# Performance work log

Measured on AMD Instinct MI355X. Metric: run time of the kernel, lower is better.

## Reference

```python
import jax, jax.numpy as jnp
import numpy as np
from jax import lax

EPS = 1e-5

def _conv(x, w, pad):
    return lax.conv_general_dilated(x, w, (1, 1), [(pad, pad), (pad, pad)],
                                    dimension_numbers=('NCHW', 'OIHW', 'NCHW'))

def _bn(x, g, b, m, v):
    inv = g * jax.lax.rsqrt(v + EPS)
    return x * inv[None, :, None, None] + (b - m * inv)[None, :, None, None]

def _deform(x, ow, ob):
    # ConvOffset2d: 3x3 conv predicts 2*C per-channel (dy,dx) offsets, then
    # bilinear resample each channel at (grid + offset), clipped to the image.
    B, C, H, W = x.shape
    off = _conv(x, ow, 1) + ob[None, :, None, None]          # [B,2C,H,W]
    off = off.reshape(B, C, 2, H, W)
    yy = jnp.arange(H, dtype=x.dtype)[:, None]
    xx = jnp.arange(W, dtype=x.dtype)[None, :]
    py = jnp.clip(yy + off[:, :, 0], 0.0, H - 1)             # [B,C,H,W]
    px = jnp.clip(xx + off[:, :, 1], 0.0, W - 1)
    y0 = jnp.floor(py).astype(jnp.int32)
    x0 = jnp.floor(px).astype(jnp.int32)
    y1 = jnp.minimum(y0 + 1, H - 1)
    x1 = jnp.minimum(x0 + 1, W - 1)
    wy = py - y0.astype(x.dtype)
    wx = px - x0.astype(x.dtype)
    flat = x.reshape(B, C, H * W)
    def g(yi, xi):
        idx = (yi * W + xi).reshape(B, C, H * W)
        return jnp.take_along_axis(flat, idx, axis=2).reshape(B, C, H, W)
    v00, v01, v10, v11 = g(y0, x0), g(y0, x1), g(y1, x0), g(y1, x1)
    return (v00 * (1 - wy) * (1 - wx) + v01 * (1 - wy) * wx +
            v10 * wy * (1 - wx) + v11 * wy * wx)

def setup_inputs() -> dict:
    key = jax.random.key(0)
    ks = jax.random.split(key, 32)
    B, Cin, Cmid, H, W = 4, 1024, 256, 64, 64
    d = {}
    d['x'] = jax.random.normal(ks[0], (B, Cin, H, W), jnp.float32)
    # offset-predicting convs (3x3, C -> 2C), small init so offsets ~O(1)
    d['ow1'] = jax.random.normal(ks[1], (2 * Cin, Cin, 3, 3), jnp.float32) * 0.01
    d['ob1'] = jnp.zeros((2 * Cin,), jnp.float32)
    d['ow2'] = jax.random.normal(ks[2], (2 * Cmid, Cmid, 3, 3), jnp.float32) * 0.01
    d['ob2'] = jnp.zeros((2 * Cmid,), jnp.float32)
    d['ow3'] = jax.random.normal(ks[3], (2 * Cmid, Cmid, 3, 3), jnp.float32) * 0.01
    d['ob3'] = jnp.zeros((2 * Cmid,), jnp.float32)
    # bottleneck convs (no bias, as in ResNet)
    d['w1'] = jax.random.normal(ks[4], (Cmid, Cin, 1, 1), jnp.float32) * (1.0 / np.sqrt(Cin))
    d['w2'] = jax.random.normal(ks[5], (Cmid, Cmid, 3, 3), jnp.float32) * (1.0 / np.sqrt(9 * Cmid))
    d['w3'] = jax.random.normal(ks[6], (Cin, Cmid, 1, 1), jnp.float32) * (1.0 / np.sqrt(Cmid))
    # batchnorm (inference) params
    for i, c in zip((1, 2, 3), (Cmid, Cmid, Cin)):
        d[f'g{i}'] = jnp.ones((c,), jnp.float32)
        d[f'b{i}'] = jnp.zeros((c,), jnp.float32)
        d[f'm{i}'] = jax.random.normal(ks[10 + i], (c,), jnp.float32) * 0.1
        d[f'v{i}'] = jnp.ones((c,), jnp.float32) + jax.random.uniform(ks[20 + i], (c,), jnp.float32) * 0.1
    return d

def reference(x, ow1, ob1, w1, g1, b1, m1, v1,
              ow2, ob2, w2, g2, b2, m2, v2,
              ow3, ob3, w3, g3, b3, m3, v3):
    h = _deform(x, ow1, ob1)
    h = _bn(_conv(h, w1, 0), g1, b1, m1, v1)
    h = _deform(h, ow2, ob2)
    h = _bn(_conv(h, w2, 1), g2, b2, m2, v2)
    h = _deform(h, ow3, ob3)
    h = _bn(_conv(h, w3, 0), g3, b3, m3, v3)
    return jax.nn.relu(h)
```

## Files before the change

### kernel.cpp

```cpp
#include <hip/hip_runtime.h>


typedef unsigned short u16;
typedef __bf16 bf16x8 __attribute__((ext_vector_type(8)));
typedef float f32x4 __attribute__((ext_vector_type(4)));
typedef _Float16 f16;

__device__ __forceinline__ u16 f2bf(float f) {
  unsigned u = __float_as_uint(f);
  u += 0x7fffu + ((u >> 16) & 1u);
  return (u16)(u >> 16);
}
__device__ __forceinline__ float bf2f(u16 h) { return __uint_as_float((unsigned)h << 16); }
__device__ __forceinline__ u16 f2h(float f) { f16 h = (f16)f; return __builtin_bit_cast(u16, h); }
__device__ __forceinline__ float h2f(u16 u) { return (float)__builtin_bit_cast(f16, u); }

__device__ __forceinline__ void gload16(const u16* g, u16* l) {
  __builtin_amdgcn_global_load_lds((__attribute__((address_space(1))) unsigned int*)g,
                                   (__attribute__((address_space(3))) unsigned int*)l,
                                   16, 0, 0);
}

#define VM8() asm volatile("s_waitcnt vmcnt(8)" ::: "memory")
#define VM6() asm volatile("s_waitcnt vmcnt(6)" ::: "memory")
#define VM0() asm volatile("s_waitcnt vmcnt(0)" ::: "memory")
#define BAR()                                   \
  do {                                          \
    asm volatile("" ::: "memory");              \
    __builtin_amdgcn_s_barrier();               \
    asm volatile("" ::: "memory");              \
  } while (0)
#define LGK0()                                          \
  do {                                                  \
    asm volatile("s_waitcnt lgkmcnt(0)" ::: "memory");  \
    __builtin_amdgcn_sched_barrier(0);                  \
  } while (0)
#define SB0() __builtin_amdgcn_sched_barrier(0)

__global__ __launch_bounds__(256) void zero_k(uint4* __restrict__ p, unsigned n) {
  unsigned i = blockIdx.x * 256u + threadIdx.x;
  const unsigned st = gridDim.x * 256u;
  uint4 z; z.x = 0u; z.y = 0u; z.z = 0u; z.w = 0u;
  for (; i < n; i += st) p[i] = z;
}

template <int SPLIT>
__global__ __launch_bounds__(256) void pack_w(const float* __restrict__ w,
                                              u16* __restrict__ hi, u16* __restrict__ lo,
                                              int M, int C, int T) {
  const int AK = C * T;
  const int id = blockIdx.x * 256 + threadIdx.x;
  if (id >= M * AK) return;
  const int j = id & 7;
  const int slot = (id >> 3) & 511;
  const int rest = id >> 12;
  const int steps = AK >> 5;
  const int step = rest % steps;
  const int mt = rest / steps;
  const int kg = slot >> 7, m = slot & 127;
  const int k = step * 32 + kg * 8 + j;
  const int tap = k / C;
  const int c = k - tap * C;
  const int mg = mt * 128 + m;
  const float v = w[((size_t)mg * C + c) * T + tap];
  const u16 h = f2bf(v);
  hi[id] = h;
  if (SPLIT) lo[id] = f2bf(v - bf2f(h));
}

template <int CC, int T>
__global__ __launch_bounds__(256) void pack8_w(const float* __restrict__ w,
                                               u16* __restrict__ dst, int M) {
  constexpr int KT2 = 2 * (T * CC / 64);
  const int id = blockIdx.x * 256 + threadIdx.x;
  if (id >= M * CC * T) return;
  const int j = id & 7;
  const int d = (id >> 3) & 1023;
  const int rest = id >> 13;
  const int H = rest % KT2;
  const int mt = rest / KT2;
  const int row = d >> 2, kq = d & 3;
  const int k = H * 32 + ((kq ^ ((row >> 1) & 3)) * 8) + j;
  const int tap = k / CC, c = k - tap * CC;
  const int oc = mt * 256 + row;
  dst[id] = f2bf(w[((size_t)oc * CC + c) * T + tap]);
}

__global__ __launch_bounds__(256) void prep_x(const float* __restrict__ x,
                                              u16* __restrict__ xp) {
  __shared__ float t[64][65];
  const int c0 = blockIdx.x * 64;
  const int y = blockIdx.y;
  const int b = blockIdx.z;
  const int tid = threadIdx.x;
#pragma unroll
  for (int i = 0; i < 16; ++i) {
    const int idx = i * 256 + tid;
    const int ci = idx >> 6, xi = idx & 63;
    t[ci][xi] = x[(((size_t)b * 1024 + c0 + ci) * 64 + y) * 64 + xi];
  }
  __syncthreads();
#pragma unroll
  for (int i = 0; i < 16; ++i) {
    const int idx = i * 256 + tid;
    const int xi = idx >> 6, ci = idx & 63;
    xp[((size_t)((b * 66 + y + 1) * 66 + (xi + 1))) * 1024 + c0 + ci] = f2bf(t[ci][xi]);
  }
}

template <int C, int PADDST>
__global__ __launch_bounds__(256) void deform_k(const u16* __restrict__ src,
                                                const u16* __restrict__ off,
                                                u16* __restrict__ dst) {
  const int id = blockIdx.x * 256 + threadIdx.x;
  const int c = id & (C - 1);
  const int pix = id / C;
  const int b = pix >> 12;
  const int y = (pix >> 6) & 63;
  const int x = pix & 63;
  const unsigned ov = *(const unsigned*)(off + (size_t)pix * (2 * C) + 2 * c);
  const float py = fminf(fmaxf((float)y + h2f((u16)(ov & 0xffffu)), 0.f), 63.f);
  const float px = fminf(fmaxf((float)x + h2f((u16)(ov >> 16)), 0.f), 63.f);
  const int y0i = (int)py, x0i = (int)px;
  const int y1i = min(y0i + 1, 63), x1i = min(x0i + 1, 63);
  const float wy = py - (float)y0i, wx = px - (float)x0i;
  const int bb66 = b * 66;
  auto at = [&](int yi, int xi) -> size_t {
    return ((size_t)((bb66 + yi + 1) * 66 + (xi + 1))) * C + c;
  };
  const float v00 = bf2f(src[at(y0i, x0i)]);
  const float v01 = bf2f(src[at(y0i, x1i)]);
  const float v10 = bf2f(src[at(y1i, x0i)]);
  const float v11 = bf2f(src[at(y1i, x1i)]);
  const float val = v00 * (1.f - wy) * (1.f - wx) + v01 * (1.f - wy) * wx +
                    v10 * wy * (1.f - wx) + v11 * wy * wx;
  const size_t d = PADDST ? at(y, x) : (size_t)id;
  dst[d] = f2bf(val);
}

template <int TAPS, int CC, int NMT>
__global__ __launch_bounds__(512, 2) void gemm8_conv(
    const u16* __restrict__ Apack, const u16* __restrict__ Bsrc,
    const float* __restrict__ bias, u16* __restrict__ out, int M) {
  constexpr int KT = TAPS * CC / 64;
  constexpr int KT2 = 2 * KT;
  __shared__ u16 lds[65536];
  const int tid = threadIdx.x;
  const int w = tid >> 6, lane = tid & 63;
  const int wm = w >> 2, wn = w & 3;
  const int kg = lane >> 4, lm = lane & 15;
  const int g = blockIdx.x;
  const int local = g >> 3;
  const int mt = local % NMT;
  const int nt = (g & 7) * 8 + local / NMT;
  const int b_img = nt >> 4;
  const int y0 = (nt & 15) * 4;

  int laneA[2], laneB[2];
  unsigned ldsoff[2];
#pragma unroll
  for (int it = 0; it < 2; ++it) {
    const int d = it * 512 + tid;
    laneA[it] = d * 8;
    const int pl = d >> 2, kq = d & 3;
    const int r = pl >> 6, xc = pl & 63;
    laneB[it] = (r * 66 + xc) * CC + (kq ^ ((pl >> 1) & 3)) * 8;
    ldsoff[it] = (unsigned)(it * 512 + (tid & ~63)) * 8u;
  }
  const u16* Abase = Apack + (size_t)mt * KT2 * 8192;
  const u16* Bbase = Bsrc + (size_t)(b_img * 66 + y0) * 66 * CC;

  f32x4 acc[8][4];
  const f32x4 fz = {0.f, 0.f, 0.f, 0.f};
#pragma unroll
  for (int i = 0; i < 8; ++i)
#pragma unroll
    for (int j = 0; j < 4; ++j) acc[i][j] = fz;

  auto rbase = [&](int b, int op, int kh) -> unsigned {
    return (unsigned)(((b * 2 + op) * 2 + kh) * 8192);
  };
  auto stageA = [&](int H) {
    if (H >= KT2) return;
    const u16* p = Abase + (size_t)H * 8192;
    const unsigned db = rbase((H >> 1) & 1, 0, H & 1);
    gload16(p + laneA[0], (u16*)&lds[db + ldsoff[0]]);
    gload16(p + laneA[1], (u16*)&lds[db + ldsoff[1]]);
  };
  auto stageB = [&](int H) {
    if (H >= KT2) return;
    const int kglob = H * 32;
    const int tap = (TAPS == 1) ? 0 : (kglob / CC);
    const int cbase = kglob - tap * CC;
    const int ky = (TAPS == 9) ? tap / 3 : 0, kx = (TAPS == 9) ? tap % 3 : 0;
    const u16* p = Bbase + (ky * 66 + kx) * CC + cbase;
    const unsigned db = rbase((H >> 1) & 1, 1, H & 1);
    gload16(p + laneB[0], (u16*)&lds[db + ldsoff[0]]);
    gload16(p + laneB[1], (u16*)&lds[db + ldsoff[1]]);
  };

  bf16x8 afE[4], afO[4], bfA[4], bfB[4];
  auto rdA = [&](bf16x8* dst, int buf, int kh, int MG) {
    const unsigned regA = rbase(buf, 0, kh);
#pragma unroll
    for (int f = 0; f < 4; ++f) {
      const int row = wm * 128 + (MG * 4 + f) * 16 + lm;
      dst[f] = *(const bf16x8*)&lds[regA + row * 32 + (kg ^ ((row >> 1) & 3)) * 8];
    }
  };
  auto rdB = [&](bf16x8* dst, int buf, int kh) {
    const unsigned regB = rbase(buf, 1, kh);
#pragma unroll
    for (int f = 0; f < 4; ++f) {
      const int pc = wn * 64 + f * 16 + lm;
      dst[f] = *(const bf16x8*)&lds[regB + pc * 32 + (kg ^ ((pc >> 1) & 3)) * 8];
    }
  };

#define MFMA16(MG_, AF_, BF_)                                                        \
  do {                                                                               \
    __builtin_amdgcn_s_setprio(1);                                                   \
    _Pragma("unroll") for (int f = 0; f < 4; ++f)                                    \
        _Pragma("unroll") for (int nf = 0; nf < 4; ++nf)                             \
            acc[MG_ * 4 + f][nf] = __builtin_amdgcn_mfma_f32_16x16x32_bf16(          \
                AF_[f], BF_[nf], acc[MG_ * 4 + f][nf], 0, 0, 0);                     \
    __builtin_amdgcn_s_setprio(0);                                                   \
  } while (0)

  stageA(0); stageB(0);
  stageA(1); stageB(1);
  stageA(2); stageB(2);
  VM8();
  BAR();
  rdA(afE, 0, 0, 0);
  rdB(bfA, 0, 0);

  for (int t = 0; t < KT; ++t) {
    const int bi = t & 1;
    LGK0();
    rdA(afO, bi, 0, 1);
    stageA(2 * t + 3);
    SB0();
    MFMA16(0, afE, bfA);
    if (t >= KT - 2) VM0(); else VM6();
    BAR();
    LGK0();
    rdA(afE, bi, 1, 0);
    rdB(bfB, bi, 1);
    stageB(2 * t + 3);
    SB0();
    MFMA16(1, afO, bfA);
    BAR();
    LGK0();
    rdA(afO, bi, 1, 1);
    stageA(2 * t + 4);
    SB0();
    MFMA16(0, afE, bfB);
    if (t < KT - 2) VM6();
    BAR();
    LGK0();
    if (t + 1 < KT) {
      rdA(afE, bi ^ 1, 0, 0);
      rdB(bfA, bi ^ 1, 0);
    }
    stageB(2 * t + 4);
    SB0();
    MFMA16(1, afO, bfB);
    BAR();
  }
#undef MFMA16

  const int ocb = mt * 256 + wm * 128 + kg * 4;
#pragma unroll
  for (int mf = 0; mf < 8; ++mf) {
    const int oc0 = ocb + mf * 16;
    const f32x4 bv = *(const f32x4*)&bias[oc0];
#pragma unroll
    for (int nf = 0; nf < 4; ++nf) {
      const int pix = nt * 256 + wn * 64 + nf * 16 + lm;
      f32x4 r = acc[mf][nf] + bv;
      uint2 hv;
      hv.x = (unsigned)f2h(r[0]) | ((unsigned)f2h(r[1]) << 16);
      hv.y = (unsigned)f2h(r[2]) | ((unsigned)f2h(r[3]) << 16);
      *(uint2*)(out + (size_t)pix * M + oc0) = hv;
    }
  }
}

template <int TAPS, int PAD, int EPI, int CC, int WSPLIT>
__global__ __launch_bounds__(256, 2) void gemm_conv(
    const u16* __restrict__ Aph, const u16* __restrict__ Apl,
    const u16* __restrict__ Bh,
    const float* __restrict__ p0, const float* __restrict__ p1,
    const float* __restrict__ p2, const float* __restrict__ p3,
    float* __restrict__ outF, u16* __restrict__ o16a, int M) {
  constexpr int NB = 2 + WSPLIT;
  __shared__ u16 lds[NB * 4096];
  constexpr int steps = TAPS * (CC / 32);
  const int tid = threadIdx.x;
  const int w = tid >> 6, lane = tid & 63;
  const int wm = (w >> 1) * 64, wn = (w & 1) * 64;
  const int kg = lane >> 4, lm = lane & 15;
  const int wg = blockIdx.x;
  const int chunk = (int)(gridDim.x >> 3);
  const int g = (wg & 7) * chunk + (wg >> 3);
  const int mt = g >> 7, nt = g & 127;
  const int b_img = nt >> 5;
  const int y0 = (nt & 31) * 2;

  f32x4 acc[4][4];
  const f32x4 fz = {0.f, 0.f, 0.f, 0.f};
#pragma unroll
  for (int i = 0; i < 4; ++i)
#pragma unroll
    for (int j = 0; j < 4; ++j) acc[i][j] = fz;

  const u16* Abase_h = Aph + (size_t)mt * steps * 4096;
  const u16* Abase_l = WSPLIT ? (Apl + (size_t)mt * steps * 4096) : nullptr;

  for (int step = 0; step < steps; ++step) {
    const int tap = (TAPS == 1) ? 0 : (step / (CC / 32));
    const int c0 = (step - tap * (CC / 32)) * 32;
    const int ky = (TAPS == 9) ? (tap / 3) : 0;
    const int kx = (TAPS == 9) ? (tap % 3) : 0;

#pragma unroll
    for (int it = 0; it < 2; ++it) {
      const int slot = w * 128 + it * 64 + lane;
      const unsigned ldso = (unsigned)(w * 128 + it * 64) * 8u;
      const size_t ga = (size_t)step * 4096 + (size_t)slot * 8;
      gload16(Abase_h + ga, &lds[0 * 4096 + ldso]);
      if (WSPLIT) gload16(Abase_l + ga, &lds[1 * 4096 + ldso]);
      const int n = slot >> 2, kq = slot & 3;
      const int kga = kq ^ ((n >> 1) & 3);
      size_t gb;
      if (PAD) {
        const int r = n >> 6, xc = n & 63;
        gb = ((size_t)((b_img * 66 + (y0 + r + ky)) * 66 + (xc + kx))) * CC +
             (size_t)(c0 + kga * 8);
      } else {
        gb = (size_t)(nt * 128 + n) * CC + (size_t)(c0 + kga * 8);
      }
      gload16(Bh + gb, &lds[(NB - 1) * 4096 + ldso]);
    }
    __syncthreads();

    bf16x8 ah[4], al[4], bh[4];
#pragma unroll
    for (int f = 0; f < 4; ++f) {
      const unsigned ao = (unsigned)(kg * 128 + wm + f * 16 + lm) * 8u;
      ah[f] = *(const bf16x8*)&lds[0 * 4096 + ao];
      if (WSPLIT) al[f] = *(const bf16x8*)&lds[1 * 4096 + ao];
      const int n = wn + f * 16 + lm;
      const unsigned bo = (unsigned)(n * 4 + (kg ^ ((n >> 1) & 3))) * 8u;
      bh[f] = *(const bf16x8*)&lds[(NB - 1) * 4096 + bo];
    }
#pragma unroll
    for (int i = 0; i < 4; ++i)
#pragma unroll
      for (int j = 0; j < 4; ++j) {
        acc[i][j] = __builtin_amdgcn_mfma_f32_16x16x32_bf16(ah[i], bh[j], acc[i][j], 0, 0, 0);
        if (WSPLIT)
          acc[i][j] = __builtin_amdgcn_mfma_f32_16x16x32_bf16(al[i], bh[j], acc[i][j], 0, 0, 0);
      }
    __syncthreads();
  }

  const int ocb = mt * 128 + wm + kg * 4;
#pragma unroll
  for (int fi = 0; fi < 4; ++fi) {
    const int oc0 = ocb + fi * 16;
    f32x4 scl, sft;
    if (EPI == 0) {
#pragma unroll
      for (int j = 0; j < 4; ++j) { scl[j] = 1.f; sft[j] = p0[oc0 + j]; }
    } else {
#pragma unroll
      for (int j = 0; j < 4; ++j) {
        const float inv = p0[oc0 + j] / sqrtf(p3[oc0 + j] + 1e-5f);
        scl[j] = inv;
        sft[j] = p1[oc0 + j] - p2[oc0 + j] * inv;
      }
    }
#pragma unroll
    for (int fj = 0; fj < 4; ++fj) {
      const int pix = nt * 128 + wn + fj * 16 + lm;
      f32x4 r = acc[fi][fj] * scl + sft;
      if (EPI == 0) {
        uint2 hv;
        hv.x = (unsigned)f2h(r[0]) | ((unsigned)f2h(r[1]) << 16);
        hv.y = (unsigned)f2h(r[2]) | ((unsigned)f2h(r[3]) << 16);
        *(uint2*)(o16a + (size_t)pix * M + oc0) = hv;
      } else if (EPI == 1) {
        const int bb = pix >> 12, yy = (pix >> 6) & 63, xx = pix & 63;
        const size_t pp = ((size_t)((bb * 66 + yy + 1) * 66 + (xx + 1))) * M + oc0;
        uint2 hv;
        hv.x = (unsigned)f2bf(r[0]) | ((unsigned)f2bf(r[1]) << 16);
        hv.y = (unsigned)f2bf(r[2]) | ((unsigned)f2bf(r[3]) << 16);
        *(uint2*)(o16a + pp) = hv;
      } else {
        const int bb = pix >> 12, pin = pix & 4095;
#pragma unroll
        for (int j = 0; j < 4; ++j)
          outF[((size_t)(bb * M + oc0 + j)) * 4096 + pin] = fmaxf(r[j], 0.f);
      }
    }
  }
}

extern "C" void kernel_launch(void* const* d_in, const int* in_sizes, int n_in,
                              void* d_out, int out_size, void* d_ws, size_t ws_size,
                              hipStream_t stream) {
  (void)in_sizes; (void)out_size;
  if (n_in < 22) return;
  const float* x   = (const float*)d_in[0];
  const float* ow1 = (const float*)d_in[1];
  const float* ob1 = (const float*)d_in[2];
  const float* ow2 = (const float*)d_in[3];
  const float* ob2 = (const float*)d_in[4];
  const float* ow3 = (const float*)d_in[5];
  const float* ob3 = (const float*)d_in[6];
  const float* w1  = (const float*)d_in[7];
  const float* w2  = (const float*)d_in[8];
  const float* w3  = (const float*)d_in[9];
  const float* g1 = (const float*)d_in[10], *b1 = (const float*)d_in[11];
  const float* m1 = (const float*)d_in[12], *v1 = (const float*)d_in[13];
  const float* g2 = (const float*)d_in[14], *b2 = (const float*)d_in[15];
  const float* m2 = (const float*)d_in[16], *v2 = (const float*)d_in[17];
  const float* g3 = (const float*)d_in[18], *b3 = (const float*)d_in[19];
  const float* m3 = (const float*)d_in[20], *v3 = (const float*)d_in[21];

  char* W = (char*)d_ws;
  constexpr size_t P66_1024 = 4ull * 66 * 66 * 1024 * 2;
  constexpr size_t P66_256  = 4ull * 66 * 66 * 256 * 2;
  constexpr size_t SZ_OFF1  = 4ull * 4096 * 2048 * 2;
  constexpr size_t SZ_OFF2  = 4ull * 4096 * 512 * 2;
  constexpr size_t SZ_H1    = 4ull * 4096 * 1024 * 2;
  constexpr size_t SZ_H3    = 4ull * 4096 * 256 * 2;
  constexpr size_t SZ_OW1 = 2048ull * 9216 * 2;
  constexpr size_t SZ_W1  = 256ull * 1024 * 2;
  constexpr size_t SZ_OW2 = 512ull * 2304 * 2;
  constexpr size_t SZ_W2  = 256ull * 2304 * 2;
  constexpr size_t SZ_OW3 = 512ull * 2304 * 2;
  constexpr size_t SZ_W3  = 1024ull * 256 * 2;

  constexpr size_t o_ow1h = 0;
  constexpr size_t o_xp   = o_ow1h + SZ_OW1;
  constexpr size_t o_off1 = o_xp + P66_1024;
  constexpr size_t o_t1p  = o_off1;
  constexpr size_t o_off2 = o_t1p + P66_256;
  constexpr size_t o_h2p  = o_off2 + SZ_OFF2;
  constexpr size_t o_t2p  = o_h2p + P66_256;
  static_assert(o_t2p + P66_256 <= o_off1 + SZ_OFF1, "era2 fits off1 slot");
  constexpr size_t o_h1   = o_off1 + SZ_OFF1;
  constexpr size_t o_off3 = o_h1;
  constexpr size_t o_h3   = o_off3 + SZ_OFF2;
  static_assert(o_h3 + SZ_H3 <= o_h1 + SZ_H1, "off3+h3 fit h1 slot");
  constexpr size_t o_w1h  = o_h1 + SZ_H1;
  constexpr size_t o_ow2h = o_w1h + SZ_W1;
  constexpr size_t o_w2h  = o_ow2h + SZ_OW2;
  constexpr size_t o_ow3h = o_w2h + SZ_W2;
  constexpr size_t o_w3h  = o_ow3h + SZ_OW3;
  constexpr size_t WS_NEED = o_w3h + SZ_W3;
  if (ws_size < WS_NEED) return;

  auto U = [&](size_t o) { return (u16*)(W + o); };
  auto zero = [&](size_t off, size_t bytes) {
    const unsigned n = (unsigned)(bytes / 16);
    unsigned grid = (n + 255) / 256; if (grid > 4096) grid = 4096;
    zero_k<<<grid, 256, 0, stream>>>((uint4*)(W + off), n);
  };

  {
    int n;
    n = 2048 * 9216; pack8_w<1024, 9><<<(n + 255) / 256, 256, 0, stream>>>(ow1, U(o_ow1h), 2048);
    n = 512 * 2304;  pack_w<0><<<(n + 255) / 256, 256, 0, stream>>>(ow2, U(o_ow2h), nullptr, 512, 256, 9);
    n = 512 * 2304;  pack_w<0><<<(n + 255) / 256, 256, 0, stream>>>(ow3, U(o_ow3h), nullptr, 512, 256, 9);
    n = 256 * 1024;  pack_w<0><<<(n + 255) / 256, 256, 0, stream>>>(w1, U(o_w1h), nullptr, 256, 1024, 1);
    n = 256 * 2304;  pack_w<0><<<(n + 255) / 256, 256, 0, stream>>>(w2, U(o_w2h), nullptr, 256, 256, 9);
    n = 1024 * 256;  pack_w<0><<<(n + 255) / 256, 256, 0, stream>>>(w3, U(o_w3h), nullptr, 1024, 256, 1);
  }

  zero(o_xp, P66_1024);
  prep_x<<<dim3(16, 64, 4), 256, 0, stream>>>(x, U(o_xp));

  gemm8_conv<9, 1024, 8><<<512, 512, 0, stream>>>(
      U(o_ow1h), U(o_xp), ob1, U(o_off1), 2048);
  deform_k<1024, 0><<<65536, 256, 0, stream>>>(U(o_xp), U(o_off1), U(o_h1));

  zero(o_t1p, P66_256);
  zero(o_h2p, 2 * P66_256);
  gemm_conv<1, 0, 1, 1024, 0><<<256, 256, 0, stream>>>(
      U(o_w1h), nullptr, U(o_h1), g1, b1, m1, v1, nullptr, U(o_t1p), 256);
  gemm_conv<9, 1, 0, 256, 0><<<512, 256, 0, stream>>>(
      U(o_ow2h), nullptr, U(o_t1p), ob2, nullptr, nullptr, nullptr,
      nullptr, U(o_off2), 512);
  deform_k<256, 1><<<16384, 256, 0, stream>>>(U(o_t1p), U(o_off2), U(o_h2p));
  gemm_conv<9, 1, 1, 256, 0><<<256, 256, 0, stream>>>(
      U(o_w2h), nullptr, U(o_h2p), g2, b2, m2, v2, nullptr, U(o_t2p), 256);
  gemm_conv<9, 1, 0, 256, 0><<<512, 256, 0, stream>>>(
      U(o_ow3h), nullptr, U(o_t2p), ob3, nullptr, nullptr, nullptr,
      nullptr, U(o_off3), 512);
  deform_k<256, 0><<<16384, 256, 0, stream>>>(U(o_t2p), U(o_off3), U(o_h3));
  gemm_conv<1, 0, 2, 256, 0><<<1024, 256, 0, stream>>>(
      U(o_w3h), nullptr, U(o_h3), g3, b3, m3, v3, (float*)d_out, nullptr, 1024);
}
```

Measured before the change: 1.056 ms.

## Use 32x32 MFMA in offset conv, fuse prep kernels, zero only pad borders

The big offset-prediction GEMM switches from 16x16x32 to 32x32x16 bf16 MFMA tiles, reorganising the fragment loads and epilogue to match the new accumulator layout. All weight packing, input transpose and padding zeroing are merged into one launch. Full-buffer zeroing of padded activation buffers is replaced by kernels that write only the one-pixel border. This cuts launch count and memset traffic and may raise MFMA throughput, at the cost of more register pressure per accumulator and less contiguous bias loads in the epilogue.

```diff
diff --git a/kernel.cpp b/kernel.cpp
--- a/kernel.cpp
+++ b/kernel.cpp
@@ -4,6 +4,7 @@
 typedef unsigned short u16;
 typedef __bf16 bf16x8 __attribute__((ext_vector_type(8)));
 typedef float f32x4 __attribute__((ext_vector_type(4)));
+typedef float f32x16 __attribute__((ext_vector_type(16)));
 typedef _Float16 f16;
 
 __device__ __forceinline__ u16 f2bf(float f) {
@@ -37,20 +38,9 @@
   } while (0)
 #define SB0() __builtin_amdgcn_sched_barrier(0)
 
-__global__ __launch_bounds__(256) void zero_k(uint4* __restrict__ p, unsigned n) {
-  unsigned i = blockIdx.x * 256u + threadIdx.x;
-  const unsigned st = gridDim.x * 256u;
-  uint4 z; z.x = 0u; z.y = 0u; z.z = 0u; z.w = 0u;
-  for (; i < n; i += st) p[i] = z;
-}
-
-template <int SPLIT>
-__global__ __launch_bounds__(256) void pack_w(const float* __restrict__ w,
-                                              u16* __restrict__ hi, u16* __restrict__ lo,
-                                              int M, int C, int T) {
+__device__ __forceinline__ void d_pack_w(const float* __restrict__ w, u16* __restrict__ hi,
+                                         int C, int T, int id) {
   const int AK = C * T;
-  const int id = blockIdx.x * 256 + threadIdx.x;
-  if (id >= M * AK) return;
   const int j = id & 7;
   const int slot = (id >> 3) & 511;
   const int rest = id >> 12;
@@ -62,18 +52,13 @@
   const int tap = k / C;
   const int c = k - tap * C;
   const int mg = mt * 128 + m;
-  const float v = w[((size_t)mg * C + c) * T + tap];
-  const u16 h = f2bf(v);
-  hi[id] = h;
-  if (SPLIT) lo[id] = f2bf(v - bf2f(h));
-}
-
-template <int CC, int T>
-__global__ __launch_bounds__(256) void pack8_w(const float* __restrict__ w,
-                                               u16* __restrict__ dst, int M) {
+  hi[id] = f2bf(w[((size_t)mg * C + c) * T + tap]);
+}
+
+__device__ __forceinline__ void d_pack8_ow1(const float* __restrict__ w, u16* __restrict__ dst,
+                                            int id) {
+  constexpr int CC = 1024, T = 9;
   constexpr int KT2 = 2 * (T * CC / 64);
-  const int id = blockIdx.x * 256 + threadIdx.x;
-  if (id >= M * CC * T) return;
   const int j = id & 7;
   const int d = (id >> 3) & 1023;
   const int rest = id >> 13;
@@ -86,26 +71,75 @@
   dst[id] = f2bf(w[((size_t)oc * CC + c) * T + tap]);
 }
 
-__global__ __launch_bounds__(256) void prep_x(const float* __restrict__ x,
-                                              u16* __restrict__ xp) {
+__global__ __launch_bounds__(256) void mega_prep(
+    const float* __restrict__ x, u16* __restrict__ xp,
+    const float* __restrict__ ow1, u16* __restrict__ dow1,
+    const float* __restrict__ w1, u16* __restrict__ dw1,
+    const float* __restrict__ ow2, u16* __restrict__ dow2,
+    const float* __restrict__ w2, u16* __restrict__ dw2,
+    const float* __restrict__ ow3, u16* __restrict__ dow3,
+    const float* __restrict__ w3, u16* __restrict__ dw3) {
   __shared__ float t[64][65];
-  const int c0 = blockIdx.x * 64;
-  const int y = blockIdx.y;
-  const int b = blockIdx.z;
+  const int bb = blockIdx.x;
   const int tid = threadIdx.x;
-#pragma unroll
-  for (int i = 0; i < 16; ++i) {
-    const int idx = i * 256 + tid;
-    const int ci = idx >> 6, xi = idx & 63;
-    t[ci][xi] = x[(((size_t)b * 1024 + c0 + ci) * 64 + y) * 64 + xi];
+  if (bb < 4096) {
+    const int c0 = (bb & 15) * 64;
+    const int y = (bb >> 4) & 63;
+    const int b = bb >> 10;
+#pragma unroll
+    for (int i = 0; i < 16; ++i) {
+      const int idx = i * 256 + tid;
+      const int ci = idx >> 6, xi = idx & 63;
+      t[ci][xi] = x[(((size_t)b * 1024 + c0 + ci) * 64 + y) * 64 + xi];
+    }
+    __syncthreads();
+#pragma unroll
+    for (int i = 0; i < 16; ++i) {
+      const int idx = i * 256 + tid;
+      const int xi = idx >> 6, ci = idx & 63;
+      xp[((size_t)((b * 66 + y + 1) * 66 + (xi + 1))) * 1024 + c0 + ci] = f2bf(t[ci][xi]);
+    }
+  } else if (bb < 8256) {
+    const int id = (bb - 4096) * 256 + tid;
+    const int c = id & 1023;
+    const int p = id >> 10;
+    const int b = p / 260;
+    const int pi = p - b * 260;
+    int y, xx;
+    if (pi < 66) { y = 0; xx = pi; }
+    else if (pi < 132) { y = 65; xx = pi - 66; }
+    else { const int q = pi - 132; y = 1 + (q >> 1); xx = (q & 1) * 65; }
+    xp[((size_t)((b * 66 + y) * 66 + xx)) * 1024 + c] = 0;
+  } else if (bb < 81984) {
+    d_pack8_ow1(ow1, dow1, (bb - 8256) * 256 + tid);
+  } else if (bb < 83008) {
+    d_pack_w(w1, dw1, 1024, 1, (bb - 81984) * 256 + tid);
+  } else if (bb < 87616) {
+    d_pack_w(ow2, dow2, 256, 9, (bb - 83008) * 256 + tid);
+  } else if (bb < 89920) {
+    d_pack_w(w2, dw2, 256, 9, (bb - 87616) * 256 + tid);
+  } else if (bb < 94528) {
+    d_pack_w(ow3, dow3, 256, 9, (bb - 89920) * 256 + tid);
+  } else {
+    d_pack_w(w3, dw3, 256, 1, (bb - 94528) * 256 + tid);
   }
-  __syncthreads();
-#pragma unroll
-  for (int i = 0; i < 16; ++i) {
-    const int idx = i * 256 + tid;
-    const int xi = idx >> 6, ci = idx & 63;
-    xp[((size_t)((b * 66 + y + 1) * 66 + (xi + 1))) * 1024 + c0 + ci] = f2bf(t[ci][xi]);
-  }
+}
+
+__global__ __launch_bounds__(256) void border3_k(u16* __restrict__ b0, u16* __restrict__ b1,
+                                                 u16* __restrict__ b2) {
+  const int id = blockIdx.x * 256 + threadIdx.x;
+  const int buf = id / 266240;
+  const int rem = id - buf * 266240;
+  const int c = rem & 255;
+  const int p = rem >> 8;
+  const int b = p / 260;
+  const int pi = p - b * 260;
+  int y, xx;
+  if (pi < 66) { y = 0; xx = pi; }
+  else if (pi < 132) { y = 65; xx = pi - 66; }
+  else { const int q = pi - 132; y = 1 + (q >> 1); xx = (q & 1) * 65; }
+  u16* dst = buf == 0 ? b0 : (buf == 1 ? b1 : b2);
+  dst[((size_t)((b * 66 + y) * 66 + xx)) * 256 + c] = 0;
 }
 
 template <int C, int PADDST>
@@ -148,7 +182,7 @@
   const int tid = threadIdx.x;
   const int w = tid >> 6, lane = tid & 63;
   const int wm = w >> 2, wn = w & 3;
-  const int kg = lane >> 4, lm = lane & 15;
+  const int l31 = lane & 31, l5 = lane >> 5;
   const int g = blockIdx.x;
   const int local = g >> 3;
   const int mt = local % NMT;
@@ -170,12 +204,13 @@
   const u16* Abase = Apack + (size_t)mt * KT2 * 8192;
   const u16* Bbase = Bsrc + (size_t)(b_img * 66 + y0) * 66 * CC;
 
-  f32x4 acc[8][4];
-  const f32x4 fz = {0.f, 0.f, 0.f, 0.f};
-#pragma unroll
-  for (int i = 0; i < 8; ++i)
-#pragma unroll
-    for (int j = 0; j < 4; ++j) acc[i][j] = fz;
+  f32x16 acc[4][2];
+#pragma unroll
+  for (int i = 0; i < 4; ++i)
+#pragma unroll
+    for (int j = 0; j < 2; ++j)
+#pragma unroll
+      for (int e = 0; e < 16; ++e) acc[i][j][e] = 0.f;
 
   auto rbase = [&](int b, int op, int kh) -> unsigned {
     return (unsigned)(((b * 2 + op) * 2 + kh) * 8192);
@@ -200,30 +235,41 @@
   };
 
   bf16x8 afE[4], afO[4], bfA[4], bfB[4];
-  auto rdA = [&](bf16x8* dst, int buf, int kh, int MG) {
+  auto rdA = [&](bf16x8* dst, int buf, int kh, int tmsel) {
     const unsigned regA = rbase(buf, 0, kh);
 #pragma unroll
-    for (int f = 0; f < 4; ++f) {
-      const int row = wm * 128 + (MG * 4 + f) * 16 + lm;
-      dst[f] = *(const bf16x8*)&lds[regA + row * 32 + (kg ^ ((row >> 1) & 3)) * 8];
-    }
+    for (int tm2 = 0; tm2 < 2; ++tm2)
+#pragma unroll
+      for (int ks = 0; ks < 2; ++ks) {
+        const int row = wm * 128 + (tmsel * 2 + tm2) * 32 + l31;
+        const int kq = ks * 2 + l5;
+        dst[tm2 * 2 + ks] =
+            *(const bf16x8*)&lds[regA + row * 32 + (kq ^ ((row >> 1) & 3)) * 8];
+      }
   };
   auto rdB = [&](bf16x8* dst, int buf, int kh) {
     const unsigned regB = rbase(buf, 1, kh);
 #pragma unroll
-    for (int f = 0; f < 4; ++f) {
-      const int pc = wn * 64 + f * 16 + lm;
-      dst[f] = *(const bf16x8*)&lds[regB + pc * 32 + (kg ^ ((pc >> 1) & 3)) * 8];
-    }
+    for (int tn = 0; tn < 2; ++tn)
+#pragma unroll
+      for (int ks = 0; ks < 2; ++ks) {
+        const int p = wn * 64 + tn * 32 + l31;
+        const int kq = ks * 2 + l5;
+        dst[tn * 2 + ks] =
+            *(const bf16x8*)&lds[regB + p * 32 + (kq ^ ((p >> 1) & 3)) * 8];
+      }
   };
 
-#define MFMA16(MG_, AF_, BF_)                                                        \
+#define MFMA8(TMSEL_, AF_, BF_)                                                      \
   do {                                                                               \
     __builtin_amdgcn_s_setprio(1);                                                   \
-    _Pragma("unroll") for (int f = 0; f < 4; ++f)                                    \
-        _Pragma("unroll") for (int nf = 0; nf < 4; ++nf)                             \
-            acc[MG_ * 4 + f][nf] = __builtin_amdgcn_mfma_f32_16x16x32_bf16(          \
-                AF_[f], BF_[nf], acc[MG_ * 4 + f][nf], 0, 0, 0);                     \
+    _Pragma("unroll") for (int tm2 = 0; tm2 < 2; ++tm2)                              \
+        _Pragma("unroll") for (int tn = 0; tn < 2; ++tn) {                           \
+      acc[TMSEL_ * 2 + tm2][tn] = __builtin_amdgcn_mfma_f32_32x32x16_bf16(           \
+          AF_[tm2 * 2 + 0], BF_[tn * 2 + 0], acc[TMSEL_ * 2 + tm2][tn], 0, 0, 0);    \
+      acc[TMSEL_ * 2 + tm2][tn] = __builtin_amdgcn_mfma_f32_32x32x16_bf16(           \
+          AF_[tm2 * 2 + 1], BF_[tn * 2 + 1], acc[TMSEL_ * 2 + tm2][tn], 0, 0, 0);    \
+    }                                                                                \
     __builtin_amdgcn_s_setprio(0);                                                   \
   } while (0)
 
@@ -241,7 +287,7 @@
     rdA(afO, bi, 0, 1);
     stageA(2 * t + 3);
     SB0();
-    MFMA16(0, afE, bfA);
+    MFMA8(0, afE, bfA);
     if (t >= KT - 2) VM0(); else VM6();
     BAR();
     LGK0();
@@ -249,13 +295,13 @@
     rdB(bfB, bi, 1);
     stageB(2 * t + 3);
     SB0();
-    MFMA16(1, afO, bfA);
+    MFMA8(1, afO, bfA);
     BAR();
     LGK0();
     rdA(afO, bi, 1, 1);
     stageA(2 * t + 4);
     SB0();
-    MFMA16(0, afE, bfB);
+    MFMA8(0, afE, bfB);
     if (t < KT - 2) VM6();
     BAR();
     LGK0();
@@ -265,26 +311,29 @@
     }
     stageB(2 * t + 4);
     SB0();
-    MFMA16(1, afO, bfB);
+    MFMA8(1, afO, bfB);
     BAR();
   }
-#undef MFMA16
-
-  const int ocb = mt * 256 + wm * 128 + kg * 4;
-#pragma unroll
-  for (int mf = 0; mf < 8; ++mf) {
-    const int oc0 = ocb + mf * 16;
-    const f32x4 bv = *(const f32x4*)&bias[oc0];
-#pragma unroll
-    for (int nf = 0; nf < 4; ++nf) {
-      const int pix = nt * 256 + wn * 64 + nf * 16 + lm;
-      f32x4 r = acc[mf][nf] + bv;
-      uint2 hv;
-      hv.x = (unsigned)f2h(r[0]) | ((unsigned)f2h(r[1]) << 16);
-      hv.y = (unsigned)f2h(r[2]) | ((unsigned)f2h(r[3]) << 16);
-      *(uint2*)(out + (size_t)pix * M + oc0) = hv;
-    }
-  }
+#undef MFMA8
+
+#pragma unroll
+  for (int tm = 0; tm < 4; ++tm)
+#pragma unroll
+    for (int tn = 0; tn < 2; ++tn) {
+      const int pix = nt * 256 + wn * 64 + tn * 32 + l31;
+#pragma unroll
+      for (int q = 0; q < 4; ++q) {
+        const int oc0 = mt * 256 + wm * 128 + tm * 32 + q * 8 + l5 * 4;
+        float r0 = acc[tm][tn][q * 4 + 0] + bias[oc0 + 0];
+        float r1 = acc[tm][tn][q * 4 + 1] + bias[oc0 + 1];
+        float r2 = acc[tm][tn][q * 4 + 2] + bias[oc0 + 2];
+        float r3 = acc[tm][tn][q * 4 + 3] + bias[oc0 + 3];
+        uint2 hv;
+        hv.x = (unsigned)f2h(r0) | ((unsigned)f2h(r1) << 16);
+        hv.y = (unsigned)f2h(r2) | ((unsigned)f2h(r3) << 16);
+        *(uint2*)(out + (size_t)pix * M + oc0) = hv;
+      }
+    }
 }
 
 template <int TAPS, int PAD, int EPI, int CC, int WSPLIT>
@@ -465,31 +514,16 @@
   if (ws_size < WS_NEED) return;
 
   auto U = [&](size_t o) { return (u16*)(W + o); };
-  auto zero = [&](size_t off, size_t bytes) {
-    const unsigned n = (unsigned)(bytes / 16);
-    unsigned grid = (n + 255) / 256; if (grid > 4096) grid = 4096;
-    zero_k<<<grid, 256, 0, stream>>>((uint4*)(W + off), n);
-  };
-
-  {
-    int n;
-    n = 2048 * 9216; pack8_w<1024, 9><<<(n + 255) / 256, 256, 0, stream>>>(ow1, U(o_ow1h), 2048);
-    n = 512 * 2304;  pack_w<0><<<(n + 255) / 256, 256, 0, stream>>>(ow2, U(o_ow2h), nullptr, 512, 256, 9);
-    n = 512 * 2304;  pack_w<0><<<(n + 255) / 256, 256, 0, stream>>>(ow3, U(o_ow3h), nullptr, 512, 256, 9);
-    n = 256 * 1024;  pack_w<0><<<(n + 255) / 256, 256, 0, stream>>>(w1, U(o_w1h), nullptr, 256, 1024, 1);
-    n = 256 * 2304;  pack_w<0><<<(n + 255) / 256, 256, 0, stream>>>(w2, U(o_w2h), nullptr, 256, 256, 9);
-    n = 1024 * 256;  pack_w<0><<<(n + 255) / 256, 256, 0, stream>>>(w3, U(o_w3h), nullptr, 1024, 256, 1);
-  }
-
-  zero(o_xp, P66_1024);
-  prep_x<<<dim3(16, 64, 4), 256, 0, stream>>>(x, U(o_xp));
+
+  mega_prep<<<95552, 256, 0, stream>>>(
+      x, U(o_xp), ow1, U(o_ow1h), w1, U(o_w1h), ow2, U(o_ow2h),
+      w2, U(o_w2h), ow3, U(o_ow3h), w3, U(o_w3h));
 
   gemm8_conv<9, 1024, 8><<<512, 512, 0, stream>>>(
       U(o_ow1h), U(o_xp), ob1, U(o_off1), 2048);
   deform_k<1024, 0><<<65536, 256, 0, stream>>>(U(o_xp), U(o_off1), U(o_h1));
 
-  zero(o_t1p, P66_256);
-  zero(o_h2p, 2 * P66_256);
+  border3_k<<<3120, 256, 0, stream>>>(U(o_t1p), U(o_h2p), U(o_t2p));
   gemm_conv<1, 0, 1, 1024, 0><<<256, 256, 0, stream>>>(
       U(o_w1h), nullptr, U(o_h1), g1, b1, m1, v1, nullptr, U(o_t1p), 256);
   gemm_conv<9, 1, 0, 256, 0><<<512, 256, 0, stream>>>(
```

Measured after the change: 1.106 ms. 4.7% more time.
